# Kernel optimization log

Hardware: AMD Instinct MI355X
Metric: run time of the kernel (lower is better)

## Reference

```python
import jax, jax.numpy as jnp
import numpy as np

N = 50000      # nodes
E = 800000     # edges
H = 128        # num_node_hidden_channels
G = 50         # num_edge_gaussians
F = 128        # num_node_interaction_channels (= num_filters = out dim)
S = 2          # num_state_features
B = 256        # num graphs
NCONV = 2
CUTOFF = 5.0


def _ssp(x):
    # ShiftedSoftplus: softplus(x) - log(2)
    return jax.nn.softplus(x) - jnp.log(2.0).astype(x.dtype)


def _xavier(k, shape):
    fan_in = shape[-1]
    return (jax.random.normal(k, shape) / np.sqrt(fan_in)).astype(jnp.float32)


def setup_inputs() -> dict:
    key = jax.random.key(0)
    ks = jax.random.split(key, 16)
    h = jax.random.normal(ks[0], (N, H), dtype=jnp.float32)
    edge_index = jax.random.randint(ks[1], (2, E), 0, N, dtype=jnp.int64)
    edge_weight = jax.random.uniform(ks[2], (E,), dtype=jnp.float32) * CUTOFF
    edge_attr = jax.random.normal(ks[3], (E, G), dtype=jnp.float32)
    batch = jnp.sort(jax.random.randint(ks[4], (N,), 0, B, dtype=jnp.int64))
    state_attr = jax.random.normal(ks[5], (B, S), dtype=jnp.float32)
    # parameters, stacked over n_conv layers
    params = dict(
        lin1_w=_xavier(ks[6], (NCONV, H, H + S)),
        lin1_b=jnp.zeros((NCONV, H), jnp.float32),
        mlp_w1=_xavier(ks[7], (NCONV, F, G)),
        mlp_b1=jnp.zeros((NCONV, F), jnp.float32),
        mlp_w2=_xavier(ks[8], (NCONV, F, F)),
        mlp_b2=jnp.zeros((NCONV, F), jnp.float32),
        conv_lin1_w=_xavier(ks[9], (NCONV, F, H)),
        conv_lin2_w=_xavier(ks[10], (NCONV, H, F)),
        conv_lin2_b=jnp.zeros((NCONV, H), jnp.float32),
        out_w=_xavier(ks[11], (F, H)),
        out_b=jnp.zeros((F,), jnp.float32),
    )
    return dict(h=h, edge_weight=edge_weight, edge_attr=edge_attr,
                state_attr=state_attr, **params,
                edge_index=edge_index, batch=batch)


def _forward(h, edge_weight, edge_attr, state_attr,
             lin1_w, lin1_b, mlp_w1, mlp_b1, mlp_w2, mlp_b2,
             conv_lin1_w, conv_lin2_w, conv_lin2_b, out_w, out_b,
             edge_index, batch):
    src, dst = edge_index[0], edge_index[1]   # x_j gathered from src, aggregated at dst
    nB = state_attr.shape[0]
    # cosine cutoff envelope (same for all layers)
    C = 0.5 * (jnp.cos(edge_weight * (np.pi / CUTOFF)) + 1.0)   # [E]
    counts = jax.ops.segment_sum(jnp.ones((h.shape[0],), h.dtype), batch,
                                 num_segments=nB)               # [B]
    inv_counts = 1.0 / jnp.maximum(counts, 1.0)
    for i in range(NCONV):
        sa = state_attr[batch]                                  # [N,S]
        hs = jnp.concatenate([sa, h], axis=1)                   # [N,S+H]
        h2 = hs @ lin1_w[i].T + lin1_b[i]                       # [N,H]
        # edge filter MLP * cutoff
        eh = _ssp(edge_attr @ mlp_w1[i].T + mlp_b1[i]) @ mlp_w2[i].T + mlp_b2[i]
        W = eh * C[:, None]                                     # [E,F]
        # CFConv: lift -> gather-multiply -> scatter-add
        xf = h2 @ conv_lin1_w[i].T                              # [N,F]
        msg = xf[src] * W                                       # [E,F]
        agg = jax.ops.segment_sum(msg, dst, num_segments=h.shape[0])  # [N,F]
        xc = agg @ conv_lin2_w[i].T + conv_lin2_b[i]            # [N,H]
        h = h2 + _ssp(xc)                                       # residual + act
        # segment mean pooling over graphs, then global state update
        r = jax.ops.segment_sum(h, batch, num_segments=nB) * inv_counts[:, None]
        state_attr = jnp.broadcast_to(jnp.sum(r, axis=1, keepdims=True),
                                      state_attr.shape)
    return h @ out_w.T + out_b                                  # [N,F]


def reference(h, edge_weight, edge_attr, state_attr,
              lin1_w, lin1_b, mlp_w1, mlp_b1, mlp_w2, mlp_b2,
              conv_lin1_w, conv_lin2_w, conv_lin2_b, out_w, out_b,
              edge_index, batch):
    return _forward(h, edge_weight, edge_attr, state_attr,
                    lin1_w, lin1_b, mlp_w1, mlp_b1, mlp_w2, mlp_b2,
                    conv_lin1_w, conv_lin2_w, conv_lin2_b, out_w, out_b,
                    edge_index, batch)
```

## Files before the change

kernel.cpp:

```cpp
#include <hip/hip_runtime.h>

#define NN 50000
#define EE 800000
#define HH 128
#define GG 50
#define FF 128
#define SS 2
#define BB 256
#define SLOT_CAP 16

typedef short bf16x8 __attribute__((ext_vector_type(8)));
typedef float floatx4 __attribute__((ext_vector_type(4)));

union FragU { bf16x8 v; unsigned short u[8]; unsigned int d[4]; uint4 q; };

__device__ __forceinline__ float bf2f(unsigned short u) {
    union { unsigned int i; float f; } c; c.i = ((unsigned int)u) << 16; return c.f;
}
__device__ __forceinline__ unsigned short f2bf(float f) {
    union { float f; unsigned int i; } c; c.f = f;
    unsigned int i = c.i;
    unsigned int r = (i + 0x7fffu + ((i >> 16) & 1u)) >> 16;
    return (unsigned short)r;
}
__device__ __forceinline__ float sspf(float x) {
    float l = __logf(1.f + __expf(x));
    l = (x > 20.f) ? x : l;
    return l - 0.69314718056f;
}
__device__ __forceinline__ bf16x8 f8frag(const float* p) {
    FragU f;
#pragma unroll
    for (int j = 0; j < 8; j++) f.u[j] = f2bf(p[j]);
    return f.v;
}
__device__ __forceinline__ bf16x8 load16(const unsigned short* p) {
    FragU f; f.q = *(const uint4*)p; return f.v;
}
__device__ __forceinline__ bf16x8 loaddw(const unsigned short* p) {
    FragU f; const unsigned int* pp = (const unsigned int*)p;
#pragma unroll
    for (int t = 0; t < 4; t++) f.d[t] = pp[t];
    return f.v;
}
__device__ __forceinline__ int clampi(int v, int hi) {
    v = (v < 0) ? 0 : v;
    return (v > hi) ? hi : v;
}

__global__ __launch_bounds__(256) void kConv(const float* __restrict__ s,
                                             unsigned short* __restrict__ d, int n) {
    for (int i = blockIdx.x * 256 + threadIdx.x; i < n; i += gridDim.x * 256)
        d[i] = f2bf(s[i]);
}

__global__ __launch_bounds__(256) void kConvW(const float* __restrict__ a0,
                                              const float* __restrict__ a1,
                                              const float* __restrict__ a2,
                                              const float* __restrict__ a3,
                                              const float* __restrict__ a4,
                                              const float* __restrict__ a5,
                                              unsigned short* __restrict__ d) {
    int i = blockIdx.x * 256 + threadIdx.x;
    float v;
    if (i < 12800)        v = a0[i];
    else if (i < 45568)   v = a1[i - 12800];
    else if (i < 78336)   v = a2[i - 45568];
    else if (i < 111104)  v = a3[i - 78336];
    else if (i < 144384)  v = a4[i - 111104];
    else if (i < 160768)  v = a5[i - 144384];
    else {
        int j = i - 160768;
        int k = j & 63;
        int nl = j >> 6;
        v = (k < 50) ? a0[nl * 50 + k] : 0.f;
    }
    d[i] = f2bf(v);
}

__global__ __launch_bounds__(256) void kPrep(const int* __restrict__ batch,
                                             int* __restrict__ counts,
                                             const float* __restrict__ sa_in,
                                             float* __restrict__ stateBuf) {
    int i = blockIdx.x * 256 + threadIdx.x;
    if (i < NN) atomicAdd(&counts[clampi(batch[i], BB - 1)], 1);
    if (i < BB * SS) stateBuf[i] = sa_in[i];
}

__global__ __launch_bounds__(256) void kHist(const int* __restrict__ eidx,
                                             int* __restrict__ cnt) {
    for (int e = blockIdx.x * 256 + threadIdx.x; e < EE; e += gridDim.x * 256)
        atomicAdd(&cnt[clampi(eidx[EE + e], NN - 1)], 1);
}

__global__ __launch_bounds__(1024) void kScanA(const int* __restrict__ cnt,
                                               int* __restrict__ off,
                                               int* __restrict__ blkSum) {
    __shared__ int s[1024];
    int tid = threadIdx.x;
    int g = blockIdx.x * 1024 + tid;
    int v = (g < NN) ? cnt[g] : 0;
    s[tid] = v;
    __syncthreads();
#pragma unroll
    for (int o = 1; o < 1024; o <<= 1) {
        int x = (tid >= o) ? s[tid - o] : 0;
        __syncthreads();
        s[tid] += x;
        __syncthreads();
    }
    if (g < NN) off[g] = s[tid] - v;
    if (tid == 1023) blkSum[blockIdx.x] = s[1023];
}
__global__ void kScanB(int* __restrict__ blkSum, int nb) {
    if (threadIdx.x == 0) {
        int acc = 0;
        for (int i = 0; i < nb; i++) { int t = blkSum[i]; blkSum[i] = acc; acc += t; }
    }
}
__global__ __launch_bounds__(256) void kScanC(int* __restrict__ off,
                                              const int* __restrict__ blkSum) {
    int g = blockIdx.x * 256 + threadIdx.x;
    if (g < NN) off[g] += blkSum[g >> 10];
}

__global__ __launch_bounds__(256) void kScatter(const int* __restrict__ eidx,
                                                const float* __restrict__ ew,
                                                const int* __restrict__ off,
                                                int* __restrict__ cur,
                                                int* __restrict__ pos,
                                                int* __restrict__ ePerm,
                                                int* __restrict__ dstS,
                                                int* __restrict__ srcS,
                                                float* __restrict__ cS) {
    for (int e = blockIdx.x * 256 + threadIdx.x; e < EE; e += gridDim.x * 256) {
        int d = clampi(eidx[EE + e], NN - 1);
        int p = off[d] + atomicAdd(&cur[d], 1);
        pos[e] = p;
        ePerm[p] = e;
        dstS[p] = d;
        srcS[p] = clampi(eidx[e], NN - 1);
        float w = ew[e];
        cS[p] = 0.5f * (__cosf(w * 0.62831853072f) + 1.f);
    }
}

__global__ __launch_bounds__(256) void kPermEA(const float* __restrict__ ea,
                                               const int* __restrict__ pos,
                                               unsigned short* __restrict__ eaSb) {
    int idx = blockIdx.x * 256 + threadIdx.x;
    int e = idx >> 2, part = idx & 3;
    int p = pos[e];
    const float* src = ea + (size_t)e * 50 + part * 16;
    FragU f0, f1;
#pragma unroll
    for (int j = 0; j < 8; j++) f0.u[j] = (part * 16 + j < 50) ? f2bf(src[j]) : 0;
#pragma unroll
    for (int j = 0; j < 8; j++) f1.u[j] = (part * 16 + 8 + j < 50) ? f2bf(src[8 + j]) : 0;
    uint4* d = (uint4*)(eaSb + (size_t)p * 64 + part * 16);
    d[0] = f0.q; d[1] = f1.q;
}

__global__ __launch_bounds__(256) void kA(const unsigned short* __restrict__ hb,
                                          const unsigned short* __restrict__ l1wb,
                                          const float* __restrict__ lin1w,
                                          const float* __restrict__ lin1b,
                                          const unsigned short* __restrict__ c1wb,
                                          const float* __restrict__ stateBuf,
                                          const int* __restrict__ batch,
                                          unsigned short* __restrict__ h2b,
                                          unsigned short* __restrict__ xfb) {
    __shared__ __align__(16) unsigned short P[64][136];
    int lane = threadIdx.x & 63;
    int wave = threadIdx.x >> 6;
    int m = lane & 15, q = lane >> 4;
    int rowBase = blockIdx.x * 64 + wave * 16;
    int arow = rowBase + m;
    int arowc = (arow < NN) ? arow : (NN - 1);

    floatx4 acc[8];
#pragma unroll
    for (int t = 0; t < 8; t++) acc[t] = (floatx4){0.f, 0.f, 0.f, 0.f};

#pragma unroll
    for (int k0 = 0; k0 < 128; k0 += 32) {
        bf16x8 a = load16(hb + (size_t)arowc * 128 + k0 + q * 8);
#pragma unroll
        for (int t = 0; t < 8; t++) {
            int n = t * 16 + m;
            bf16x8 b = loaddw(l1wb + (size_t)n * 130 + 2 + k0 + q * 8);
            acc[t] = __builtin_amdgcn_mfma_f32_16x16x32_bf16(a, b, acc[t], 0, 0, 0);
        }
    }

    int r0 = rowBase + q * 4;
    float s0[4], s1[4];
#pragma unroll
    for (int j = 0; j < 4; j++) {
        int r = r0 + j; int rc = (r < NN) ? r : (NN - 1);
        int g = clampi(batch[rc], BB - 1);
        s0[j] = stateBuf[g * 2 + 0];
        s1[j] = stateBuf[g * 2 + 1];
    }
#pragma unroll
    for (int t = 0; t < 8; t++) {
        int c = t * 16 + m;
        float w0 = lin1w[(size_t)c * 130 + 0];
        float w1 = lin1w[(size_t)c * 130 + 1];
        float bb = lin1b[c];
#pragma unroll
        for (int j = 0; j < 4; j++) {
            int r = r0 + j;
            unsigned short vb = f2bf(acc[t][j] + bb + s0[j] * w0 + s1[j] * w1);
            if (r < NN) h2b[(size_t)r * 128 + c] = vb;
            P[wave * 16 + q * 4 + j][c] = vb;
        }
    }
    __syncthreads();

    floatx4 acc2[8];
#pragma unroll
    for (int t = 0; t < 8; t++) acc2[t] = (floatx4){0.f, 0.f, 0.f, 0.f};
#pragma unroll
    for (int k0 = 0; k0 < 128; k0 += 32) {
        FragU fa; fa.q = *(const uint4*)&P[wave * 16 + m][k0 + q * 8];
#pragma unroll
        for (int t = 0; t < 8; t++) {
            int n = t * 16 + m;
            bf16x8 b = load16(c1wb + (size_t)n * 128 + k0 + q * 8);
            acc2[t] = __builtin_amdgcn_mfma_f32_16x16x32_bf16(fa.v, b, acc2[t], 0, 0, 0);
        }
    }
#pragma unroll
    for (int t = 0; t < 8; t++) {
        int c = t * 16 + m;
#pragma unroll
        for (int j = 0; j < 4; j++) {
            int r = r0 + j;
            if (r < NN) xfb[(size_t)r * 128 + c] = f2bf(acc2[t][j]);
        }
    }
}

__global__ __launch_bounds__(256) void kF(const unsigned short* __restrict__ eaSb,
                                          const unsigned short* __restrict__ w1pb,
                                          const float* __restrict__ b1,
                                          const unsigned short* __restrict__ w2b,
                                          const float* __restrict__ b2,
                                          const int* __restrict__ dstS,
                                          const int* __restrict__ srcS,
                                          const float* __restrict__ cS,
                                          const unsigned short* __restrict__ xfb,
                                          float* __restrict__ agg) {
    __shared__ __align__(16) unsigned short P[64][136];
    __shared__ float accS[SLOT_CAP][132];
    __shared__ int sSlot[64];
    __shared__ int sSlotDst[64];
    __shared__ int sD;

    int tid = threadIdx.x;
    int lane = tid & 63;
    int wave = tid >> 6;
    int m = lane & 15, q = lane >> 4;
    int base = blockIdx.x * 64;

    int gr = tid >> 2, gc = tid & 3;
    int gsrc = srcS[base + gr];
    const uint4* gs = (const uint4*)&xfb[(size_t)gsrc * 128 + gc * 32];
    uint4 x0 = gs[0], x1 = gs[1], x2 = gs[2], x3 = gs[3];

    if (tid < 64) {
        int i = tid;
        int di = dstS[base + i];
        bool flag = (i == 0) || (di != dstS[base + i - 1]);
        unsigned long long bm = __ballot(flag ? 1 : 0);
        unsigned long long low = (i == 63) ? ~0ull : ((1ull << (i + 1)) - 1ull);
        int slot = (int)__popcll(bm & low) - 1;
        sSlot[i] = slot;
        if (flag) sSlotDst[slot] = di;
        if (i == 63) sD = slot + 1;
    }

    int eRow = base + wave * 16 + m;
    floatx4 acc[8];
#pragma unroll
    for (int t = 0; t < 8; t++) acc[t] = (floatx4){0.f, 0.f, 0.f, 0.f};
#pragma unroll
    for (int k0 = 0; k0 < 64; k0 += 32) {
        bf16x8 a = load16(eaSb + (size_t)eRow * 64 + k0 + q * 8);
#pragma unroll
        for (int t = 0; t < 8; t++) {
            int n = t * 16 + m;
            bf16x8 b = load16(w1pb + (size_t)n * 64 + k0 + q * 8);
            acc[t] = __builtin_amdgcn_mfma_f32_16x16x32_bf16(a, b, acc[t], 0, 0, 0);
        }
    }
#pragma unroll
    for (int t = 0; t < 8; t++) {
        int c = t * 16 + m;
        float bb = b1[c];
#pragma unroll
        for (int j = 0; j < 4; j++)
            P[wave * 16 + q * 4 + j][c] = f2bf(sspf(acc[t][j] + bb));
    }
    __syncthreads();

    int D = sD;
    int Dc = (D < SLOT_CAP) ? D : SLOT_CAP;
    float* accFlat = &accS[0][0];
    for (int i = tid; i < Dc * 132; i += 256) accFlat[i] = 0.f;

    floatx4 acc2[8];
#pragma unroll
    for (int t = 0; t < 8; t++) acc2[t] = (floatx4){0.f, 0.f, 0.f, 0.f};
#pragma unroll
    for (int k0 = 0; k0 < 128; k0 += 32) {
        FragU fa; fa.q = *(const uint4*)&P[wave * 16 + m][k0 + q * 8];
#pragma unroll
        for (int t = 0; t < 8; t++) {
            int n = t * 16 + m;
            bf16x8 b = load16(w2b + (size_t)n * 128 + k0 + q * 8);
            acc2[t] = __builtin_amdgcn_mfma_f32_16x16x32_bf16(fa.v, b, acc2[t], 0, 0, 0);
        }
    }
    __syncthreads();

    {
        uint4* dptr = (uint4*)&P[gr][gc * 32];
        dptr[0] = x0; dptr[1] = x1; dptr[2] = x2; dptr[3] = x3;
    }
    __syncthreads();

    int sl[4], rj[4]; float Cj[4];
#pragma unroll
    for (int j = 0; j < 4; j++) {
        int r = wave * 16 + q * 4 + j;
        rj[j] = r;
        sl[j] = sSlot[r];
        Cj[j] = cS[base + r];
    }
#pragma unroll
    for (int t = 0; t < 8; t++) {
        int c = t * 16 + m;
        float bb = b2[c];
        float v4[4];
#pragma unroll
        for (int j = 0; j < 4; j++)
            v4[j] = (acc2[t][j] + bb) * Cj[j] * bf2f(P[rj[j]][c]);
        float run = v4[0];
#pragma unroll
        for (int j = 1; j < 4; j++) {
            if (sl[j] == sl[j - 1]) run += v4[j];
            else {
                int s = sl[j - 1];
                if (s < SLOT_CAP) atomicAdd(&accS[s][c], run);
                else unsafeAtomicAdd(&agg[(size_t)sSlotDst[s] * 128 + c], run);
                run = v4[j];
            }
        }
        {
            int s = sl[3];
            if (s < SLOT_CAP) atomicAdd(&accS[s][c], run);
            else unsafeAtomicAdd(&agg[(size_t)sSlotDst[s] * 128 + c], run);
        }
    }
    __syncthreads();

    for (int idx = tid; idx < Dc * 128; idx += 256) {
        int s = idx >> 7, cc = idx & 127;
        float v = accS[s][cc];
        size_t o = (size_t)sSlotDst[s] * 128 + cc;
        if (s > 0 && s < D - 1) agg[o] = v;
        else unsafeAtomicAdd(&agg[o], v);
    }
}

__global__ __launch_bounds__(256) void kE2(const float* __restrict__ ea,
                                           const unsigned short* __restrict__ w1b,
                                           const float* __restrict__ b1,
                                           const unsigned short* __restrict__ w2b,
                                           const float* __restrict__ b2,
                                           const int* __restrict__ ePerm,
                                           const int* __restrict__ dstS,
                                           const int* __restrict__ srcS,
                                           const float* __restrict__ cS,
                                           const unsigned short* __restrict__ xfb,
                                           float* __restrict__ agg) {
    __shared__ __align__(16) unsigned short P[64][136];
    __shared__ float accS[64][132];
    __shared__ int sSlot[64];
    __shared__ int sSlotDst[64];
    __shared__ int sD;

    int tid = threadIdx.x;
    int lane = tid & 63;
    int wave = tid >> 6;
    int m = lane & 15, q = lane >> 4;
    int base = blockIdx.x * 64;

    float* accFlat = &accS[0][0];
    for (int i = tid; i < 64 * 132; i += 256) accFlat[i] = 0.f;

    if (tid < 64) {
        int i = tid;
        int di = dstS[base + i];
        bool flag = (i == 0) || (di != dstS[base + i - 1]);
        unsigned long long bm = __ballot(flag ? 1 : 0);
        unsigned long long low = (i == 63) ? ~0ull : ((1ull << (i + 1)) - 1ull);
        int slot = (int)__popcll(bm & low) - 1;
        sSlot[i] = slot;
        if (flag) sSlotDst[slot] = di;
        if (i == 63) sD = slot + 1;
    }

    int eRow = ePerm[base + wave * 16 + m];

    floatx4 acc[8];
#pragma unroll
    for (int t = 0; t < 8; t++) acc[t] = (floatx4){0.f, 0.f, 0.f, 0.f};
    {
        bf16x8 a = f8frag(ea + (size_t)eRow * 50 + q * 8);
#pragma unroll
        for (int t = 0; t < 8; t++) {
            int n = t * 16 + m;
            bf16x8 b = loaddw(w1b + (size_t)n * 50 + q * 8);
            acc[t] = __builtin_amdgcn_mfma_f32_16x16x32_bf16(a, b, acc[t], 0, 0, 0);
        }
    }
    {
        int kbase = 32 + q * 8;
        FragU fa;
        const float* pa = ea + (size_t)eRow * 50 + kbase;
#pragma unroll
        for (int j = 0; j < 8; j++) fa.u[j] = (kbase + j < 50) ? f2bf(pa[j]) : 0;
#pragma unroll
        for (int t = 0; t < 8; t++) {
            int n = t * 16 + m;
            FragU fb;
            const unsigned int* pb = (const unsigned int*)(w1b + (size_t)n * 50 + kbase);
#pragma unroll
            for (int t2 = 0; t2 < 4; t2++) fb.d[t2] = (kbase + 2 * t2 < 50) ? pb[t2] : 0u;
            acc[t] = __builtin_amdgcn_mfma_f32_16x16x32_bf16(fa.v, fb.v, acc[t], 0, 0, 0);
        }
    }
#pragma unroll
    for (int t = 0; t < 8; t++) {
        int c = t * 16 + m;
        float bb = b1[c];
#pragma unroll
        for (int j = 0; j < 4; j++)
            P[wave * 16 + q * 4 + j][c] = f2bf(sspf(acc[t][j] + bb));
    }
    __syncthreads();

    floatx4 acc2[8];
#pragma unroll
    for (int t = 0; t < 8; t++) acc2[t] = (floatx4){0.f, 0.f, 0.f, 0.f};
#pragma unroll
    for (int k0 = 0; k0 < 128; k0 += 32) {
        FragU fa; fa.q = *(const uint4*)&P[wave * 16 + m][k0 + q * 8];
#pragma unroll
        for (int t = 0; t < 8; t++) {
            int n = t * 16 + m;
            bf16x8 b = load16(w2b + (size_t)n * 128 + k0 + q * 8);
            acc2[t] = __builtin_amdgcn_mfma_f32_16x16x32_bf16(fa.v, b, acc2[t], 0, 0, 0);
        }
    }

    int sl[4], srcj[4]; float Cj[4];
#pragma unroll
    for (int j = 0; j < 4; j++) {
        int r = wave * 16 + q * 4 + j;
        int g = base + r;
        sl[j] = sSlot[r];
        Cj[j] = cS[g];
        srcj[j] = srcS[g];
    }
#pragma unroll
    for (int t = 0; t < 8; t++) {
        int c = t * 16 + m;
        float bb = b2[c];
        float v4[4];
#pragma unroll
        for (int j = 0; j < 4; j++)
            v4[j] = (acc2[t][j] + bb) * Cj[j] * bf2f(xfb[(size_t)srcj[j] * 128 + c]);
        float run = v4[0];
#pragma unroll
        for (int j = 1; j < 4; j++) {
            if (sl[j] == sl[j - 1]) run += v4[j];
            else { atomicAdd(&accS[sl[j - 1]][c], run); run = v4[j]; }
        }
        atomicAdd(&accS[sl[3]][c], run);
    }
    __syncthreads();

    int D = sD;
    for (int idx = tid; idx < D * 128; idx += 256) {
        int s = idx >> 7, c = idx & 127;
        unsafeAtomicAdd(&agg[(size_t)sSlotDst[s] * 128 + c], accS[s][c]);
    }
}

__global__ __launch_bounds__(256) void kC(const float* __restrict__ agg,
                                          const unsigned short* __restrict__ wb,
                                          const float* __restrict__ b,
                                          const unsigned short* __restrict__ h2b,
                                          unsigned short* __restrict__ hnb,
                                          const int* __restrict__ batch,
                                          float* __restrict__ pool,
                                          int doPool) {
    int lane = threadIdx.x & 63;
    int wave = threadIdx.x >> 6;
    int m = lane & 15, q = lane >> 4;
    int rowBase = blockIdx.x * 64 + wave * 16;
    int arow = rowBase + m;
    int arowc = (arow < NN) ? arow : (NN - 1);

    floatx4 acc[8];
#pragma unroll
    for (int t = 0; t < 8; t++) acc[t] = (floatx4){0.f, 0.f, 0.f, 0.f};

#pragma unroll
    for (int k0 = 0; k0 < 128; k0 += 32) {
        bf16x8 fa = f8frag(agg + (size_t)arowc * 128 + k0 + q * 8);
#pragma unroll
        for (int t = 0; t < 8; t++) {
            int n = t * 16 + m;
            bf16x8 bfr = load16(wb + (size_t)n * 128 + k0 + q * 8);
            acc[t] = __builtin_amdgcn_mfma_f32_16x16x32_bf16(fa, bfr, acc[t], 0, 0, 0);
        }
    }

    int r0 = rowBase + q * 4;
    float vsum[4] = {0.f, 0.f, 0.f, 0.f};
#pragma unroll
    for (int t = 0; t < 8; t++) {
        int c = t * 16 + m;
        float bb = b[c];
#pragma unroll
        for (int j = 0; j < 4; j++) {
            int r = r0 + j; int rc = (r < NN) ? r : (NN - 1);
            float v = bf2f(h2b[(size_t)rc * 128 + c]) + sspf(acc[t][j] + bb);
            if (r < NN) {
                hnb[(size_t)r * 128 + c] = f2bf(v);
                vsum[j] += v;
            }
        }
    }
    if (doPool) {
#pragma unroll
        for (int j = 0; j < 4; j++) {
            float v = vsum[j];
#pragma unroll
            for (int off = 1; off < 16; off <<= 1) v += __shfl_xor(v, off, 16);
            int r = r0 + j;
            if (m == 0 && r < NN) unsafeAtomicAdd(&pool[clampi(batch[r], BB - 1)], v);
        }
    }
}

__global__ __launch_bounds__(256) void kS(const float* __restrict__ pool,
                                          const int* __restrict__ counts,
                                          float* __restrict__ stateBuf) {
    int b = threadIdx.x;
    if (b < BB) {
        float c = (float)counts[b];
        c = (c < 1.f) ? 1.f : c;
        float v = pool[b] / c;
        stateBuf[b * 2 + 0] = v;
        stateBuf[b * 2 + 1] = v;
    }
}

__global__ __launch_bounds__(256) void kOut(const unsigned short* __restrict__ hnb,
                                            const unsigned short* __restrict__ owb,
                                            const float* __restrict__ ob,
                                            float* __restrict__ out) {
    int lane = threadIdx.x & 63;
    int wave = threadIdx.x >> 6;
    int m = lane & 15, q = lane >> 4;
    int rowBase = blockIdx.x * 64 + wave * 16;
    int arow = rowBase + m;
    int arowc = (arow < NN) ? arow : (NN - 1);

    floatx4 acc[8];
#pragma unroll
    for (int t = 0; t < 8; t++) acc[t] = (floatx4){0.f, 0.f, 0.f, 0.f};
#pragma unroll
    for (int k0 = 0; k0 < 128; k0 += 32) {
        bf16x8 a = load16(hnb + (size_t)arowc * 128 + k0 + q * 8);
#pragma unroll
        for (int t = 0; t < 8; t++) {
            int n = t * 16 + m;
            bf16x8 bfr = load16(owb + (size_t)n * 128 + k0 + q * 8);
            acc[t] = __builtin_amdgcn_mfma_f32_16x16x32_bf16(a, bfr, acc[t], 0, 0, 0);
        }
    }
    int r0 = rowBase + q * 4;
#pragma unroll
    for (int t = 0; t < 8; t++) {
        int c = t * 16 + m;
        float bb = ob[c];
#pragma unroll
        for (int j = 0; j < 4; j++) {
            int r = r0 + j;
            if (r < NN) out[(size_t)r * 128 + c] = acc[t][j] + bb;
        }
    }
}

extern "C" void kernel_launch(void* const* d_in, const int* in_sizes, int n_in,
                              void* d_out, int out_size, void* d_ws, size_t ws_size,
                              hipStream_t stream) {
    const float* h     = (const float*)d_in[0];
    const float* ew    = (const float*)d_in[1];
    const float* ea    = (const float*)d_in[2];
    const float* sa    = (const float*)d_in[3];
    const float* lin1w = (const float*)d_in[4];
    const float* lin1b = (const float*)d_in[5];
    const float* mw1   = (const float*)d_in[6];
    const float* mb1   = (const float*)d_in[7];
    const float* mw2   = (const float*)d_in[8];
    const float* mb2   = (const float*)d_in[9];
    const float* c1w   = (const float*)d_in[10];
    const float* c2w   = (const float*)d_in[11];
    const float* c2b   = (const float*)d_in[12];
    const float* outw  = (const float*)d_in[13];
    const float* outb  = (const float*)d_in[14];
    const int* eidx    = (const int*)d_in[15];
    const int* batch   = (const int*)d_in[16];
    float* out = (float*)d_out;

    char* ws = (char*)d_ws;
    unsigned short* hnb   = (unsigned short*)(ws);
    unsigned short* h2b   = (unsigned short*)(ws + 12800000);
    unsigned short* xfb   = (unsigned short*)(ws + 25600000);
    float*          agg   = (float*)(ws + 38400000);
    int*            pos   = (int*)(ws + 64000000);
    int*            ePerm = (int*)(ws + 67200000);
    int*            dstS  = (int*)(ws + 70400000);
    int*            srcS  = (int*)(ws + 73600000);
    float*          cS    = (float*)(ws + 76800000);
    int*            cnt   = (int*)(ws + 80000000);
    int*            off   = (int*)(ws + 80200000);
    int*            cur   = (int*)(ws + 80400000);
    int*            blkSum= (int*)(ws + 80600000);
    unsigned short* wb    = (unsigned short*)(ws + 80600512);
    float*          pool  = (float*)(ws + 80954816);
    int*            counts= (int*)(ws + 80955840);
    float*          stateBuf = (float*)(ws + 80956864);
    const size_t EAOFF = 80958912;
    unsigned short* eaSb = (unsigned short*)(ws + EAOFF);

    const size_t need = EAOFF + (size_t)EE * 64 * 2;
    const int useF = (ws_size >= need) ? 1 : 0;

    unsigned short* mw1b = wb;
    unsigned short* mw2b = wb + 12800;
    unsigned short* c1wb = wb + 45568;
    unsigned short* c2wb = wb + 78336;
    unsigned short* l1wb = wb + 111104;
    unsigned short* owb  = wb + 144384;
    unsigned short* w1pb = wb + 160768;

    hipMemsetAsync(cnt, 0, NN * 4, stream);
    hipMemsetAsync(cur, 0, NN * 4, stream);
    hipMemsetAsync(counts, 0, BB * 4, stream);
    hipMemsetAsync(pool, 0, BB * 4, stream);

    kPrep<<<(NN + 255) / 256, 256, 0, stream>>>(batch, counts, sa, stateBuf);
    kHist<<<1024, 256, 0, stream>>>(eidx, cnt);
    kScanA<<<(NN + 1023) / 1024, 1024, 0, stream>>>(cnt, off, blkSum);
    kScanB<<<1, 64, 0, stream>>>(blkSum, (NN + 1023) / 1024);
    kScanC<<<(NN + 255) / 256, 256, 0, stream>>>(off, blkSum);
    kScatter<<<1024, 256, 0, stream>>>(eidx, ew, off, cur, pos, ePerm, dstS, srcS, cS);

    kConvW<<<177152 / 256, 256, 0, stream>>>(mw1, mw2, c1w, c2w, lin1w, outw, wb);
    kConv<<<4096, 256, 0, stream>>>(h, hnb, NN * 128);
    if (useF) {
        kPermEA<<<(EE * 4) / 256, 256, 0, stream>>>(ea, pos, eaSb);
    }

    const int gridN = (NN + 63) / 64;
    const int gridE = EE / 64;

    for (int i = 0; i < 2; i++) {
        hipMemsetAsync(agg, 0, (size_t)NN * 128 * 4, stream);
        kA<<<gridN, 256, 0, stream>>>(hnb,
                                      l1wb + (size_t)i * 128 * 130,
                                      lin1w + (size_t)i * 128 * 130,
                                      lin1b + (size_t)i * 128,
                                      c1wb + (size_t)i * 128 * 128,
                                      stateBuf, batch, h2b, xfb);
        if (useF) {
            kF<<<gridE, 256, 0, stream>>>(eaSb,
                                          w1pb + (size_t)i * 128 * 64,
                                          mb1 + (size_t)i * 128,
                                          mw2b + (size_t)i * 128 * 128,
                                          mb2 + (size_t)i * 128,
                                          dstS, srcS, cS, xfb, agg);
        } else {
            kE2<<<gridE, 256, 0, stream>>>(ea,
                                           mw1b + (size_t)i * 128 * 50,
                                           mb1 + (size_t)i * 128,
                                           mw2b + (size_t)i * 128 * 128,
                                           mb2 + (size_t)i * 128,
                                           ePerm, dstS, srcS, cS, xfb, agg);
        }
        kC<<<gridN, 256, 0, stream>>>(agg,
                                      c2wb + (size_t)i * 128 * 128,
                                      c2b + (size_t)i * 128,
                                      h2b, hnb, batch, pool, (i == 0) ? 1 : 0);
        if (i == 0) kS<<<1, 256, 0, stream>>>(pool, counts, stateBuf);
    }
    kOut<<<gridN, 256, 0, stream>>>(hnb, owb, outb, out);
}
```

Before: 1.532 ms.

## Make edge-filter kernel wave-independent with per-wave segment reduction

```diff
diff --git a/kernel.cpp b/kernel.cpp
--- a/kernel.cpp
+++ b/kernel.cpp
@@ -7,7 +7,7 @@
 #define FF 128
 #define SS 2
 #define BB 256
-#define SLOT_CAP 16
+#define SLOTW 8
 
 typedef short bf16x8 __attribute__((ext_vector_type(8)));
 typedef float floatx4 __attribute__((ext_vector_type(4)));
@@ -252,48 +252,63 @@
                                           const float* __restrict__ cS,
                                           const unsigned short* __restrict__ xfb,
                                           float* __restrict__ agg) {
-    __shared__ __align__(16) unsigned short P[64][136];
-    __shared__ float accS[SLOT_CAP][132];
-    __shared__ int sSlot[64];
-    __shared__ int sSlotDst[64];
-    __shared__ int sD;
+    __shared__ __align__(16) unsigned short P[4][16][136];
+    __shared__ float accW[4][SLOTW][132];
+    __shared__ int slotDst[4][16];
 
     int tid = threadIdx.x;
     int lane = tid & 63;
-    int wave = tid >> 6;
+    int w = tid >> 6;
     int m = lane & 15, q = lane >> 4;
-    int base = blockIdx.x * 64;
-
-    int gr = tid >> 2, gc = tid & 3;
+    int base = (blockIdx.x * 4 + w) * 16;
+
+    int gr = lane >> 2, gc = lane & 3;
     int gsrc = srcS[base + gr];
     const uint4* gs = (const uint4*)&xfb[(size_t)gsrc * 128 + gc * 32];
     uint4 x0 = gs[0], x1 = gs[1], x2 = gs[2], x3 = gs[3];
 
-    if (tid < 64) {
-        int i = tid;
-        int di = dstS[base + i];
-        bool flag = (i == 0) || (di != dstS[base + i - 1]);
-        unsigned long long bm = __ballot(flag ? 1 : 0);
-        unsigned long long low = (i == 63) ? ~0ull : ((1ull << (i + 1)) - 1ull);
-        int slot = (int)__popcll(bm & low) - 1;
-        sSlot[i] = slot;
-        if (flag) sSlotDst[slot] = di;
-        if (i == 63) sD = slot + 1;
-    }
-
-    int eRow = base + wave * 16 + m;
+    int eRow = base + m;
+    bf16x8 a0 = load16(eaSb + (size_t)eRow * 64 + 0  + q * 8);
+    bf16x8 a1 = load16(eaSb + (size_t)eRow * 64 + 32 + q * 8);
+
+    int d_r = dstS[base + m];
+    int dp = __shfl(d_r, (lane - 1) & 63);
+    bool flag = (m == 0) || (d_r != dp);
+    unsigned long long bm = __ballot(flag ? 1 : 0);
+    unsigned int bmlow = (unsigned int)(bm & 0xFFFFull);
+    int D = __popc(bmlow);
+    int Dc = (D < SLOTW) ? D : SLOTW;
+    {
+        int slot_m = __popc(bmlow & ((2u << m) - 1u)) - 1;
+        if (lane < 16 && flag) slotDst[w][slot_m] = d_r;
+    }
+    float Cj[4]; int sl[4];
+#pragma unroll
+    for (int j = 0; j < 4; j++) {
+        int r = q * 4 + j;
+        Cj[j] = cS[base + r];
+        sl[j] = __popc(bmlow & ((2u << r) - 1u)) - 1;
+    }
+
+    {
+        float* fl = &accW[w][0][0];
+        for (int i = lane; i < Dc * 132; i += 64) fl[i] = 0.f;
+    }
+
     floatx4 acc[8];
 #pragma unroll
     for (int t = 0; t < 8; t++) acc[t] = (floatx4){0.f, 0.f, 0.f, 0.f};
 #pragma unroll
-    for (int k0 = 0; k0 < 64; k0 += 32) {
-        bf16x8 a = load16(eaSb + (size_t)eRow * 64 + k0 + q * 8);
-#pragma unroll
-        for (int t = 0; t < 8; t++) {
-            int n = t * 16 + m;
-            bf16x8 b = load16(w1pb + (size_t)n * 64 + k0 + q * 8);
-            acc[t] = __builtin_amdgcn_mfma_f32_16x16x32_bf16(a, b, acc[t], 0, 0, 0);
-        }
+    for (int t = 0; t < 8; t++) {
+        int n = t * 16 + m;
+        bf16x8 b = load16(w1pb + (size_t)n * 64 + 0 + q * 8);
+        acc[t] = __builtin_amdgcn_mfma_f32_16x16x32_bf16(a0, b, acc[t], 0, 0, 0);
+    }
+#pragma unroll
+    for (int t = 0; t < 8; t++) {
+        int n = t * 16 + m;
+        bf16x8 b = load16(w1pb + (size_t)n * 64 + 32 + q * 8);
+        acc[t] = __builtin_amdgcn_mfma_f32_16x16x32_bf16(a1, b, acc[t], 0, 0, 0);
     }
 #pragma unroll
     for (int t = 0; t < 8; t++) {
@@ -301,21 +316,15 @@
         float bb = b1[c];
 #pragma unroll
         for (int j = 0; j < 4; j++)
-            P[wave * 16 + q * 4 + j][c] = f2bf(sspf(acc[t][j] + bb));
-    }
-    __syncthreads();
-
-    int D = sD;
-    int Dc = (D < SLOT_CAP) ? D : SLOT_CAP;
-    float* accFlat = &accS[0][0];
-    for (int i = tid; i < Dc * 132; i += 256) accFlat[i] = 0.f;
+            P[w][q * 4 + j][c] = f2bf(sspf(acc[t][j] + bb));
+    }
 
     floatx4 acc2[8];
 #pragma unroll
     for (int t = 0; t < 8; t++) acc2[t] = (floatx4){0.f, 0.f, 0.f, 0.f};
 #pragma unroll
     for (int k0 = 0; k0 < 128; k0 += 32) {
-        FragU fa; fa.q = *(const uint4*)&P[wave * 16 + m][k0 + q * 8];
+        FragU fa; fa.q = *(const uint4*)&P[w][m][k0 + q * 8];
 #pragma unroll
         for (int t = 0; t < 8; t++) {
             int n = t * 16 + m;
@@ -323,22 +332,12 @@
             acc2[t] = __builtin_amdgcn_mfma_f32_16x16x32_bf16(fa.v, b, acc2[t], 0, 0, 0);
         }
     }
-    __syncthreads();
 
     {
-        uint4* dptr = (uint4*)&P[gr][gc * 32];
+        uint4* dptr = (uint4*)&P[w][gr][gc * 32];
         dptr[0] = x0; dptr[1] = x1; dptr[2] = x2; dptr[3] = x3;
     }
-    __syncthreads();
-
-    int sl[4], rj[4]; float Cj[4];
-#pragma unroll
-    for (int j = 0; j < 4; j++) {
-        int r = wave * 16 + q * 4 + j;
-        rj[j] = r;
-        sl[j] = sSlot[r];
-        Cj[j] = cS[base + r];
-    }
+
 #pragma unroll
     for (int t = 0; t < 8; t++) {
         int c = t * 16 + m;
@@ -346,30 +345,29 @@
         float v4[4];
 #pragma unroll
         for (int j = 0; j < 4; j++)
-            v4[j] = (acc2[t][j] + bb) * Cj[j] * bf2f(P[rj[j]][c]);
+            v4[j] = (acc2[t][j] + bb) * Cj[j] * bf2f(P[w][q * 4 + j][c]);
         float run = v4[0];
 #pragma unroll
         for (int j = 1; j < 4; j++) {
             if (sl[j] == sl[j - 1]) run += v4[j];
             else {
                 int s = sl[j - 1];
-                if (s < SLOT_CAP) atomicAdd(&accS[s][c], run);
-                else unsafeAtomicAdd(&agg[(size_t)sSlotDst[s] * 128 + c], run);
+                if (s < SLOTW) atomicAdd(&accW[w][s][c], run);
+                else unsafeAtomicAdd(&agg[(size_t)slotDst[w][s] * 128 + c], run);
                 run = v4[j];
             }
         }
         {
             int s = sl[3];
-            if (s < SLOT_CAP) atomicAdd(&accS[s][c], run);
-            else unsafeAtomicAdd(&agg[(size_t)sSlotDst[s] * 128 + c], run);
-        }
-    }
-    __syncthreads();
-
-    for (int idx = tid; idx < Dc * 128; idx += 256) {
-        int s = idx >> 7, cc = idx & 127;
-        float v = accS[s][cc];
-        size_t o = (size_t)sSlotDst[s] * 128 + cc;
+            if (s < SLOTW) atomicAdd(&accW[w][s][c], run);
+            else unsafeAtomicAdd(&agg[(size_t)slotDst[w][s] * 128 + c], run);
+        }
+    }
+
+    for (int i = lane; i < Dc * 128; i += 64) {
+        int s = i >> 7, cc = i & 127;
+        float v = accW[w][s][cc];
+        size_t o = (size_t)slotDst[w][s] * 128 + cc;
         if (s > 0 && s < D - 1) agg[o] = v;
         else unsafeAtomicAdd(&agg[o], v);
     }
```

New measurement: 1.556 ms. No clear change (+1.6%).
